# Kernel tuning notes

Hardware: AMD Instinct MI355X
Metric: run time of the kernel (lower is better)

## Reference

```python
import jax, jax.numpy as jnp
import numpy as np
import math

B, T, C, H = 2, 2048, 512, 8
K, DIL = 3, 1
EPS = 1e-5


def _ln(x, g, b):
    m = jnp.mean(x, axis=-1, keepdims=True)
    v = jnp.mean(jnp.square(x - m), axis=-1, keepdims=True)
    return (x - m) * jax.lax.rsqrt(v + EPS) * g + b


def setup_inputs() -> dict:
    key = jax.random.key(0)
    ks = jax.random.split(key, 12)
    s = 0.02
    return {
        "x": jax.random.normal(ks[0], (B, T, C), jnp.float32),
        "conv_w": jax.random.normal(ks[1], (C, C, K), jnp.float32) * s,  # OIH
        "conv_b": jax.random.normal(ks[2], (C,), jnp.float32) * s,
        "g1": jnp.ones((C,), jnp.float32), "b1": jnp.zeros((C,), jnp.float32),
        "qkv_w": jax.random.normal(ks[3], (C, 3 * C), jnp.float32) * s,
        "qkv_b": jax.random.normal(ks[4], (3 * C,), jnp.float32) * s,
        "proj_w": jax.random.normal(ks[5], (C, C), jnp.float32) * s,
        "proj_b": jax.random.normal(ks[6], (C,), jnp.float32) * s,
        "g2": jnp.ones((C,), jnp.float32), "b2": jnp.zeros((C,), jnp.float32),
        "ffn_w1": jax.random.normal(ks[7], (C, 2 * C), jnp.float32) * s,
        "ffn_b1": jax.random.normal(ks[8], (2 * C,), jnp.float32) * s,
        "ffn_w2": jax.random.normal(ks[9], (2 * C, C), jnp.float32) * s,
        "ffn_b2": jax.random.normal(ks[10], (C,), jnp.float32) * s,
        "g3": jnp.ones((C,), jnp.float32), "b3": jnp.zeros((C,), jnp.float32),
    }


def reference(x, conv_w, conv_b, g1, b1, qkv_w, qkv_b, proj_w, proj_b,
              g2, b2, ffn_w1, ffn_b1, ffn_w2, ffn_b2, g3, b3):
    b, t, c = x.shape
    hd = c // H
    # --- causal dilated conv (left-pad only == pad both + right-trim) ---
    pad = (K - 1) * DIL
    xc = jnp.transpose(x, (0, 2, 1))  # [B,C,T]
    conv = jax.lax.conv_general_dilated(
        xc, conv_w, window_strides=(1,), padding=[(pad, 0)],
        rhs_dilation=(DIL,), dimension_numbers=("NCH", "OIH", "NCH"))
    conv = conv + conv_b[None, :, None]
    x = _ln(x + jnp.transpose(conv, (0, 2, 1)), g1, b1)
    # --- causal self-attention ---
    qkv = (x @ qkv_w + qkv_b).reshape(b, t, 3, H, hd)
    qkv = jnp.transpose(qkv, (2, 0, 3, 1, 4))  # [3,B,H,T,hd]
    q, k, v = qkv[0], qkv[1], qkv[2]
    scores = jnp.einsum("bhqd,bhkd->bhqk", q, k) / math.sqrt(hd)
    causal = jnp.tril(jnp.ones((t, t), bool))
    scores = jnp.where(causal, scores, -jnp.inf)
    attn = jax.nn.softmax(scores, axis=-1)
    out = jnp.einsum("bhqk,bhkd->bhqd", attn, v)
    out = jnp.transpose(out, (0, 2, 1, 3)).reshape(b, t, c)
    out = out @ proj_w + proj_b
    x = _ln(x + out, g2, b2)
    # --- FFN ---
    ffn = jax.nn.relu(x @ ffn_w1 + ffn_b1) @ ffn_w2 + ffn_b2
    return _ln(x + ffn, g3, b3)
```

## Files before the change

### kernel.cpp

```cpp
#include <hip/hip_runtime.h>
#include <hip/hip_bf16.h>

#define TT 2048
#define QSC 0.18033688011112042f

typedef __attribute__((ext_vector_type(4))) float f32x4;
typedef __attribute__((ext_vector_type(8))) __bf16 bf16x8;
typedef __attribute__((ext_vector_type(4))) short short4v;
typedef __attribute__((ext_vector_type(8))) short short8v;

enum { M_CONV = 0, M_QKV = 1, M_PROJ = 2, M_FFN1 = 3, M_FFN2 = 4 };

__device__ __forceinline__ void gload16(const void* g, void* l) {
    __builtin_amdgcn_global_load_lds(
        (__attribute__((address_space(1))) void*)g,
        (__attribute__((address_space(3))) void*)l, 16, 0, 0);
}

__device__ __forceinline__ short f2bf(float f) {
    unsigned u = __float_as_uint(f);
    u = (u + 0x7fffu + ((u >> 16) & 1u)) >> 16;
    return (short)u;
}

__device__ __forceinline__ float bf2f(short s) {
    unsigned u = ((unsigned)(unsigned short)s) << 16;
    return __uint_as_float(u);
}

__global__ __launch_bounds__(256) void prep_all(
    const float* __restrict__ conv_w, const float* __restrict__ x,
    const float* __restrict__ qkv_w, const float* __restrict__ proj_w,
    const float* __restrict__ f1w, const float* __restrict__ f2w,
    short* __restrict__ cwT, short* __restrict__ xpad,
    short* __restrict__ qkvT, short* __restrict__ projT,
    short* __restrict__ f1T, short* __restrict__ f2T) {
    if (blockIdx.x < 2048) {
        int t = blockIdx.x;
        const float* src; short* dst; int K, N, lt;
        if (t < 768)       { src = qkv_w;  dst = qkvT;  K = 512;  N = 1536; lt = t; }
        else if (t < 1024) { src = proj_w; dst = projT; K = 512;  N = 512;  lt = t - 768; }
        else if (t < 1536) { src = f1w;    dst = f1T;   K = 512;  N = 1024; lt = t - 1024; }
        else               { src = f2w;    dst = f2T;   K = 1024; N = 512;  lt = t - 1536; }
        int ntn = N >> 5;
        int kt = lt / ntn, nt = lt - kt * ntn;
        int k0 = kt * 32, n0 = nt * 32;
        __shared__ float tile[32][33];
        int c = threadIdx.x & 31, r = threadIdx.x >> 5;
        #pragma unroll
        for (int i = 0; i < 4; i++)
            tile[r + i * 8][c] = src[(size_t)(k0 + r + i * 8) * N + n0 + c];
        __syncthreads();
        #pragma unroll
        for (int i = 0; i < 4; i++)
            dst[(size_t)(n0 + r + i * 8) * K + k0 + c] = f2bf(tile[c][r + i * 8]);
        return;
    }
    int idx = (blockIdx.x - 2048) * 256 + threadIdx.x;
    if (idx < 786432) {
        int tap = idx >> 18, i = (idx >> 9) & 511, o = idx & 511;
        cwT[(size_t)o * 1536 + tap * 512 + i] = f2bf(conv_w[((size_t)o * 512 + i) * 3 + tap]);
        return;
    }
    idx -= 786432;
    if (idx < 2099200) {
        int i = idx & 511, rp = idx >> 9;
        int bb = rp / 2050, rr = rp - bb * 2050;
        int t = rr - 2;
        float v = (t >= 0) ? x[((size_t)(bb << 11) + t) * 512 + i] : 0.f;
        xpad[((size_t)bb * 2050 + rr) * 512 + i] = f2bf(v);
    }
}

__global__ __launch_bounds__(512) void ln_row(const float* __restrict__ in,
                                              const float* __restrict__ g,
                                              const float* __restrict__ b,
                                              float* __restrict__ outf,
                                              short* __restrict__ outb) {
    int row = blockIdx.x * 8 + (threadIdx.x >> 6);
    int l = threadIdx.x & 63;
    const float* p = in + (size_t)row * 512 + l * 8;
    f32x4 v0 = *(const f32x4*)p;
    f32x4 v1 = *(const f32x4*)(p + 4);
    float s = 0.f, ss = 0.f;
    #pragma unroll
    for (int i = 0; i < 4; i++) { s += v0[i]; ss += v0[i] * v0[i]; }
    #pragma unroll
    for (int i = 0; i < 4; i++) { s += v1[i]; ss += v1[i] * v1[i]; }
    #pragma unroll
    for (int off = 1; off < 64; off <<= 1) {
        s  += __shfl_xor(s, off);
        ss += __shfl_xor(ss, off);
    }
    float mean = s * (1.f / 512);
    float var  = ss * (1.f / 512) - mean * mean;
    float rstd = rsqrtf(var + 1e-5f);
    f32x4 g0 = *(const f32x4*)(g + l * 8), g1 = *(const f32x4*)(g + l * 8 + 4);
    f32x4 b0 = *(const f32x4*)(b + l * 8), b1 = *(const f32x4*)(b + l * 8 + 4);
    f32x4 o0, o1;
    #pragma unroll
    for (int i = 0; i < 4; i++) {
        o0[i] = (v0[i] - mean) * rstd * g0[i] + b0[i];
        o1[i] = (v1[i] - mean) * rstd * g1[i] + b1[i];
    }
    float* q = outf + (size_t)row * 512 + l * 8;
    *(f32x4*)q = o0;
    *(f32x4*)(q + 4) = o1;
    if (outb) {
        short4v p0, p1;
        #pragma unroll
        for (int i = 0; i < 4; i++) { p0[i] = f2bf(o0[i]); p1[i] = f2bf(o1[i]); }
        *(short4v*)(outb + (size_t)row * 512 + l * 8) = p0;
        *(short4v*)(outb + (size_t)row * 512 + l * 8 + 4) = p1;
    }
}

template<int MODE>
__device__ __forceinline__ const short* a_ptr(const short* A, int m0, int r, int kk, int K) {
    if constexpr (MODE == M_CONV) {
        int row = m0 + r;
        int bb = row >> 11, t5 = row & 2047;
        int tap = kk >> 9, k2 = kk & 511;
        return A + ((size_t)(bb * 2050 + t5 + tap) * 512 + k2);
    } else {
        return A + ((size_t)(m0 + r) * K + kk);
    }
}

template<int MODE>
__global__ __launch_bounds__(128) void gemm_mfma(
    const short* __restrict__ A, const short* __restrict__ Bw,
    const float* __restrict__ bias, const float* __restrict__ res,
    void* __restrict__ Cout, short* __restrict__ vTb, int K) {
    __shared__ short As[64 * 64];
    __shared__ short Bs[64 * 64];
    const int tid = threadIdx.x;
    const int w = tid >> 6, l = tid & 63;
    const int lr = l & 15, lc = l >> 4;
    const int m0 = blockIdx.x * 64, n0 = blockIdx.y * 64;
    f32x4 acc[2][4];
    #pragma unroll
    for (int mf = 0; mf < 2; mf++)
        #pragma unroll
        for (int nf = 0; nf < 4; nf++) acc[mf][nf] = (f32x4){0.f, 0.f, 0.f, 0.f};

    for (int k0 = 0; k0 < K; k0 += 64) {
        #pragma unroll
        for (int i = 0; i < 4; i++) {
            int u = i * 128 + tid;
            int r = u >> 3, c = (u & 7) ^ (r & 7);
            gload16(a_ptr<MODE>(A, m0, r, k0 + c * 8, K), (char*)As + u * 16);
            gload16(Bw + ((size_t)(n0 + r) * K + k0 + c * 8), (char*)Bs + u * 16);
        }
        __syncthreads();
        bf16x8 af[2][2], bfv[4][2];
        #pragma unroll
        for (int mf = 0; mf < 2; mf++)
            #pragma unroll
            for (int ks = 0; ks < 2; ks++) {
                int rr = w * 32 + mf * 16 + lr;
                int cc = (ks * 4 + lc) ^ (rr & 7);
                af[mf][ks] = *(const bf16x8*)&As[rr * 64 + cc * 8];
            }
        #pragma unroll
        for (int nf = 0; nf < 4; nf++)
            #pragma unroll
            for (int ks = 0; ks < 2; ks++) {
                int rr = nf * 16 + lr;
                int cc = (ks * 4 + lc) ^ (rr & 7);
                bfv[nf][ks] = *(const bf16x8*)&Bs[rr * 64 + cc * 8];
            }
        __builtin_amdgcn_s_setprio(1);
        #pragma unroll
        for (int nf = 0; nf < 4; nf++)
            #pragma unroll
            for (int ks = 0; ks < 2; ks++)
                #pragma unroll
                for (int mf = 0; mf < 2; mf++)
                    acc[mf][nf] = __builtin_amdgcn_mfma_f32_16x16x32_bf16(
                        af[mf][ks], bfv[nf][ks], acc[mf][nf], 0, 0, 0);
        __builtin_amdgcn_s_setprio(0);
        __syncthreads();
    }
    #pragma unroll
    for (int mf = 0; mf < 2; mf++) {
        int row0 = m0 + w * 32 + mf * 16 + lc * 4;
        #pragma unroll
        for (int nf = 0; nf < 4; nf++) {
            int col = n0 + nf * 16 + lr;
            float bv = bias[col];
            if constexpr (MODE == M_CONV || MODE == M_PROJ || MODE == M_FFN2) {
                float* Cf = (float*)Cout;
                #pragma unroll
                for (int rg = 0; rg < 4; rg++) {
                    size_t off = (size_t)(row0 + rg) * 512 + col;
                    Cf[off] = acc[mf][nf][rg] + bv + res[off];
                }
            } else if constexpr (MODE == M_FFN1) {
                short* Cb = (short*)Cout;
                #pragma unroll
                for (int rg = 0; rg < 4; rg++)
                    Cb[(size_t)(row0 + rg) * 1024 + col] =
                        f2bf(fmaxf(acc[mf][nf][rg] + bv, 0.f));
            } else {
                short* Cb = (short*)Cout;
                float v[4];
                #pragma unroll
                for (int rg = 0; rg < 4; rg++) {
                    v[rg] = acc[mf][nf][rg] + bv;
                    float wv = (col < 512) ? v[rg] * QSC : v[rg];
                    Cb[(size_t)(row0 + rg) * 1536 + col] = f2bf(wv);
                }
                if (col >= 1024) {
                    int vc = col - 1024, hh = vc >> 6, dd = vc & 63;
                    int bb = row0 >> 11, t5 = row0 & 2047;
                    short4v pk = {f2bf(v[0]), f2bf(v[1]), f2bf(v[2]), f2bf(v[3])};
                    *(short4v*)&vTb[((size_t)((bb << 3) + hh) * 64 + dd) * 2048 + t5] = pk;
                }
            }
        }
    }
}

__global__ __launch_bounds__(256) void attn_part(const short* __restrict__ qkvb,
                                                 const short* __restrict__ vTb,
                                                 short* __restrict__ pO,
                                                 float* __restrict__ pML) {
    __shared__ short SM[20992];
    __bf16* SMb = (__bf16*)SM;
    const int tid = threadIdx.x;
    const int w = tid >> 6, l = tid & 63;
    const int lr = l & 15, lc = l >> 4;
    const int L = blockIdx.x;
    const int bh = L & 15;
    const int par = (L >> 4) & 1;
    const int qt = 31 - (L >> 5);
    const int b = bh >> 3, h = bh & 7;
    const int qr = w * 16, q0 = qt * 64;
    const int pbase = 16384 + w * (16 * 72);
    const int ntiles = (qt >= par) ? ((qt - par) >> 1) + 1 : 0;

    #pragma unroll
    for (int i = 0; i < 2; i++) {
        int u = i * 256 + tid, r = u >> 3, c = (u & 7) ^ (r & 7);
        gload16(qkvb + ((size_t)(b * 2048 + q0 + r) * 1536 + h * 64 + c * 8),
                (char*)&SM[16384] + u * 16);
        if (ntiles > 0) {
            gload16(qkvb + ((size_t)(b * 2048 + par * 64 + r) * 1536 + 512 + h * 64 + c * 8),
                    (char*)&SM[0] + u * 16);
            gload16(vTb + ((size_t)(bh * 64 + r) * 2048 + par * 64 + c * 8),
                    (char*)&SM[8192] + u * 16);
        }
    }
    __syncthreads();
    bf16x8 aq[2];
    #pragma unroll
    for (int ks = 0; ks < 2; ks++) {
        int rr = qr + lr;
        int cc = (lc + 4 * ks) ^ (rr & 7);
        aq[ks] = *(const bf16x8*)&SM[16384 + rr * 64 + cc * 8];
    }
    __syncthreads();

    bf16x8 onesf;
    #pragma unroll
    for (int i = 0; i < 8; i++) onesf[i] = (__bf16)1.0f;

    f32x4 o[4], lacc;
    float mst[4];
    #pragma unroll
    for (int nf = 0; nf < 4; nf++) o[nf] = (f32x4){0.f, 0.f, 0.f, 0.f};
    lacc = (f32x4){0.f, 0.f, 0.f, 0.f};
    #pragma unroll
    for (int rg = 0; rg < 4; rg++) mst[rg] = -1e30f;

    for (int s = 0; s < ntiles; s++) {
        const int kt = par + 2 * s;
        const int cur = s & 1;
        if (s + 1 < ntiles) {
            int ktn = kt + 2, nb = (cur ^ 1) * 4096;
            #pragma unroll
            for (int i = 0; i < 2; i++) {
                int u = i * 256 + tid, r = u >> 3, c = (u & 7) ^ (r & 7);
                gload16(qkvb + ((size_t)(b * 2048 + ktn * 64 + r) * 1536 + 512 + h * 64 + c * 8),
                        (char*)&SM[nb] + u * 16);
                gload16(vTb + ((size_t)(bh * 64 + r) * 2048 + ktn * 64 + c * 8),
                        (char*)&SM[8192 + nb] + u * 16);
            }
        }
        f32x4 s4[4];
        #pragma unroll
        for (int nf = 0; nf < 4; nf++) s4[nf] = (f32x4){0.f, 0.f, 0.f, 0.f};
        __builtin_amdgcn_s_setprio(1);
        #pragma unroll
        for (int nf = 0; nf < 4; nf++) {
            #pragma unroll
            for (int ks = 0; ks < 2; ks++) {
                int rr = nf * 16 + lr;
                int cc = (lc + 4 * ks) ^ (rr & 7);
                bf16x8 bk = *(const bf16x8*)&SM[cur * 4096 + rr * 64 + cc * 8];
                s4[nf] = __builtin_amdgcn_mfma_f32_16x16x32_bf16(aq[ks], bk, s4[nf], 0, 0, 0);
            }
        }
        __builtin_amdgcn_s_setprio(0);
        const bool diag = (kt == qt);
        if (diag) {
            #pragma unroll
            for (int nf = 0; nf < 4; nf++)
                #pragma unroll
                for (int rg = 0; rg < 4; rg++)
                    if (nf * 16 + lr > qr + lc * 4 + rg) s4[nf][rg] = -1e30f;
        }
        float rm[4];
        int ok = 1;
        #pragma unroll
        for (int rg = 0; rg < 4; rg++) {
            float m_ = fmaxf(fmaxf(s4[0][rg], s4[1][rg]), fmaxf(s4[2][rg], s4[3][rg]));
            m_ = fmaxf(m_, __shfl_xor(m_, 1));
            m_ = fmaxf(m_, __shfl_xor(m_, 2));
            m_ = fmaxf(m_, __shfl_xor(m_, 4));
            m_ = fmaxf(m_, __shfl_xor(m_, 8));
            rm[rg] = m_;
            ok &= (m_ <= mst[rg] + 11.5f);
        }
        if (!__all(ok)) {
            #pragma unroll
            for (int rg = 0; rg < 4; rg++) {
                float mn = fmaxf(mst[rg], rm[rg]);
                float alpha = exp2f(mst[rg] - mn);
                mst[rg] = mn;
                lacc[rg] *= alpha;
                #pragma unroll
                for (int nf = 0; nf < 4; nf++) o[nf][rg] *= alpha;
            }
        }
        #pragma unroll
        for (int rg = 0; rg < 4; rg++) {
            int prow = pbase + (lc * 4 + rg) * 72;
            SMb[prow      + lr] = (__bf16)exp2f(s4[0][rg] - mst[rg]);
            SMb[prow + 16 + lr] = (__bf16)exp2f(s4[1][rg] - mst[rg]);
            SMb[prow + 32 + lr] = (__bf16)exp2f(s4[2][rg] - mst[rg]);
            SMb[prow + 48 + lr] = (__bf16)exp2f(s4[3][rg] - mst[rg]);
        }
        bf16x8 pa[2];
        #pragma unroll
        for (int ks = 0; ks < 2; ks++)
            pa[ks] = *(const bf16x8*)&SM[pbase + lr * 72 + ks * 32 + lc * 8];
        __builtin_amdgcn_s_setprio(1);
        #pragma unroll
        for (int ks = 0; ks < 2; ks++)
            lacc = __builtin_amdgcn_mfma_f32_16x16x32_bf16(pa[ks], onesf, lacc, 0, 0, 0);
        #pragma unroll
        for (int nf = 0; nf < 4; nf++) {
            #pragma unroll
            for (int ks = 0; ks < 2; ks++) {
                int rr = nf * 16 + lr;
                int cc = (lc + 4 * ks) ^ (rr & 7);
                bf16x8 bv = *(const bf16x8*)&SM[8192 + cur * 4096 + rr * 64 + cc * 8];
                o[nf] = __builtin_amdgcn_mfma_f32_16x16x32_bf16(pa[ks], bv, o[nf], 0, 0, 0);
            }
        }
        __builtin_amdgcn_s_setprio(0);
        __syncthreads();
    }

    size_t ob = (size_t)L * 4096;
    #pragma unroll
    for (int nf = 0; nf < 4; nf++) {
        #pragma unroll
        for (int rg = 0; rg < 4; rg++) {
            int rw = qr + lc * 4 + rg;
            pO[ob + rw * 64 + nf * 16 + lr] = (ntiles > 0) ? f2bf(o[nf][rg]) : (short)0;
        }
    }
    if (lr == 0) {
        #pragma unroll
        for (int rg = 0; rg < 4; rg++) {
            int rw = qr + lc * 4 + rg;
            pML[(size_t)L * 128 + rw]      = (ntiles > 0) ? mst[rg] : -1e30f;
            pML[(size_t)L * 128 + 64 + rw] = (ntiles > 0) ? lacc[rg] : 0.f;
        }
    }
}

__global__ __launch_bounds__(256) void attn_merge(const short* __restrict__ pO,
                                                  const float* __restrict__ pML,
                                                  short* __restrict__ aout) {
    int U = blockIdx.x;
    int bh = U & 15, qt = U >> 4;
    int b = bh >> 3, h = bh & 7, q0 = qt * 64;
    int L0 = ((31 - qt) << 5) | bh;
    int L1 = L0 | 16;
    int t = threadIdx.x;
    int r = t >> 2, cs = (t & 3) * 16;
    float m0 = pML[(size_t)L0 * 128 + r], l0 = pML[(size_t)L0 * 128 + 64 + r];
    float m1 = pML[(size_t)L1 * 128 + r], l1 = pML[(size_t)L1 * 128 + 64 + r];
    float mn = fmaxf(m0, m1);
    float a0 = exp2f(m0 - mn), a1 = exp2f(m1 - mn);
    float inv = 1.f / (l0 * a0 + l1 * a1);
    #pragma unroll
    for (int half = 0; half < 2; half++) {
        int c0 = cs + half * 8;
        short8v o0 = *(const short8v*)&pO[(size_t)L0 * 4096 + r * 64 + c0];
        short8v o1 = *(const short8v*)&pO[(size_t)L1 * 4096 + r * 64 + c0];
        short8v ov;
        #pragma unroll
        for (int j = 0; j < 8; j++)
            ov[j] = f2bf((bf2f(o0[j]) * a0 + bf2f(o1[j]) * a1) * inv);
        *(short8v*)&aout[(size_t)(b * 2048 + q0 + r) * 512 + h * 64 + c0] = ov;
    }
}

extern "C" void kernel_launch(void* const* d_in, const int* in_sizes, int n_in,
                              void* d_out, int out_size, void* d_ws, size_t ws_size,
                              hipStream_t stream) {
    const float* x      = (const float*)d_in[0];
    const float* conv_w = (const float*)d_in[1];
    const float* conv_b = (const float*)d_in[2];
    const float* g1     = (const float*)d_in[3];
    const float* b1     = (const float*)d_in[4];
    const float* qkv_w  = (const float*)d_in[5];
    const float* qkv_b  = (const float*)d_in[6];
    const float* proj_w = (const float*)d_in[7];
    const float* proj_b = (const float*)d_in[8];
    const float* g2     = (const float*)d_in[9];
    const float* b2     = (const float*)d_in[10];
    const float* ffn_w1 = (const float*)d_in[11];
    const float* ffn_b1 = (const float*)d_in[12];
    const float* ffn_w2 = (const float*)d_in[13];
    const float* ffn_b2 = (const float*)d_in[14];
    const float* g3     = (const float*)d_in[15];
    const float* b3     = (const float*)d_in[16];
    float* out = (float*)d_out;

    char* p = (char*)d_ws;
    short* cwT   = (short*)p;  p += 786432 * 2;
    short* qkvT  = (short*)p;  p += 786432 * 2;
    short* projT = (short*)p;  p += 262144 * 2;
    short* f1T   = (short*)p;  p += 524288 * 2;
    short* f2T   = (short*)p;  p += 524288 * 2;
    short* xpad  = (short*)p;  p += 2099200 * 2;
    float* yb    = (float*)p;  p += 2097152 * 4;
    float* x1f   = (float*)p;  p += 2097152 * 4;
    short* x1b   = (short*)p;  p += 2097152 * 2;
    short* qkvb  = (short*)p;  p += 6291456 * 2;
    short* vTb   = (short*)p;  p += 2097152 * 2;
    short* pO    = (short*)p;  p += 4194304 * 2;
    float* pML   = (float*)p;  p += 131072 * 4;
    float* x2f     = x1f;
    short* x2b     = x1b;
    short* attnout = xpad;
    short* hb      = qkvb;

    prep_all<<<13320, 256, 0, stream>>>(conv_w, x, qkv_w, proj_w, ffn_w1, ffn_w2,
                                        cwT, xpad, qkvT, projT, f1T, f2T);
    gemm_mfma<M_CONV><<<dim3(64, 8), 128, 0, stream>>>(
        xpad, cwT, conv_b, x, yb, nullptr, 1536);
    ln_row<<<512, 512, 0, stream>>>(yb, g1, b1, x1f, x1b);
    gemm_mfma<M_QKV><<<dim3(64, 24), 128, 0, stream>>>(
        x1b, qkvT, qkv_b, nullptr, qkvb, vTb, 512);
    attn_part<<<1024, 256, 0, stream>>>(qkvb, vTb, pO, pML);
    attn_merge<<<512, 256, 0, stream>>>(pO, pML, attnout);
    gemm_mfma<M_PROJ><<<dim3(64, 8), 128, 0, stream>>>(
        attnout, projT, proj_b, x1f, yb, nullptr, 512);
    ln_row<<<512, 512, 0, stream>>>(yb, g2, b2, x2f, x2b);
    gemm_mfma<M_FFN1><<<dim3(64, 16), 128, 0, stream>>>(
        x2b, f1T, ffn_b1, nullptr, hb, nullptr, 512);
    gemm_mfma<M_FFN2><<<dim3(64, 8), 128, 0, stream>>>(
        hb, f2T, ffn_b2, x2f, yb, nullptr, 1024);
    ln_row<<<512, 512, 0, stream>>>(yb, g3, b3, out, nullptr);
}
```

Baseline: 135.6 us.

## Fuse attention merge into proj GEMM A-load and store intermediates in bf16

Removes the separate attn_merge kernel. The proj GEMM now merges the two partial attention outputs, using their max and sum statistics, while staging its A tile into shared memory. All residual and pre-LayerNorm intermediates (yb, x1, x2) are stored as bf16 instead of fp32, which roughly halves their memory traffic and drops one launch. The costs are lower residual precision and a synchronous register-path A load in the proj GEMM instead of async global-to-LDS loads.

```diff
diff --git a/kernel.cpp b/kernel.cpp
--- a/kernel.cpp
+++ b/kernel.cpp
@@ -72,21 +72,21 @@
     }
 }
 
-__global__ __launch_bounds__(512) void ln_row(const float* __restrict__ in,
+__global__ __launch_bounds__(512) void ln_row(const short* __restrict__ in,
                                               const float* __restrict__ g,
                                               const float* __restrict__ b,
                                               float* __restrict__ outf,
                                               short* __restrict__ outb) {
     int row = blockIdx.x * 8 + (threadIdx.x >> 6);
     int l = threadIdx.x & 63;
-    const float* p = in + (size_t)row * 512 + l * 8;
-    f32x4 v0 = *(const f32x4*)p;
-    f32x4 v1 = *(const f32x4*)(p + 4);
+    short8v v = *(const short8v*)(in + (size_t)row * 512 + l * 8);
+    float vf[8];
     float s = 0.f, ss = 0.f;
     #pragma unroll
-    for (int i = 0; i < 4; i++) { s += v0[i]; ss += v0[i] * v0[i]; }
-    #pragma unroll
-    for (int i = 0; i < 4; i++) { s += v1[i]; ss += v1[i] * v1[i]; }
+    for (int i = 0; i < 8; i++) {
+        vf[i] = bf2f(v[i]);
+        s += vf[i]; ss += vf[i] * vf[i];
+    }
     #pragma unroll
     for (int off = 1; off < 64; off <<= 1) {
         s  += __shfl_xor(s, off);
@@ -97,21 +97,22 @@
     float rstd = rsqrtf(var + 1e-5f);
     f32x4 g0 = *(const f32x4*)(g + l * 8), g1 = *(const f32x4*)(g + l * 8 + 4);
     f32x4 b0 = *(const f32x4*)(b + l * 8), b1 = *(const f32x4*)(b + l * 8 + 4);
-    f32x4 o0, o1;
+    float ov[8];
     #pragma unroll
     for (int i = 0; i < 4; i++) {
-        o0[i] = (v0[i] - mean) * rstd * g0[i] + b0[i];
-        o1[i] = (v1[i] - mean) * rstd * g1[i] + b1[i];
-    }
-    float* q = outf + (size_t)row * 512 + l * 8;
-    *(f32x4*)q = o0;
-    *(f32x4*)(q + 4) = o1;
+        ov[i]     = (vf[i]     - mean) * rstd * g0[i] + b0[i];
+        ov[i + 4] = (vf[i + 4] - mean) * rstd * g1[i] + b1[i];
+    }
+    if (outf) {
+        float* q = outf + (size_t)row * 512 + l * 8;
+        *(f32x4*)q       = (f32x4){ov[0], ov[1], ov[2], ov[3]};
+        *(f32x4*)(q + 4) = (f32x4){ov[4], ov[5], ov[6], ov[7]};
+    }
     if (outb) {
-        short4v p0, p1;
-        #pragma unroll
-        for (int i = 0; i < 4; i++) { p0[i] = f2bf(o0[i]); p1[i] = f2bf(o1[i]); }
-        *(short4v*)(outb + (size_t)row * 512 + l * 8) = p0;
-        *(short4v*)(outb + (size_t)row * 512 + l * 8 + 4) = p1;
+        short8v pk;
+        #pragma unroll
+        for (int i = 0; i < 8; i++) pk[i] = f2bf(ov[i]);
+        *(short8v*)(outb + (size_t)row * 512 + l * 8) = pk;
     }
 }
 
@@ -130,8 +131,9 @@
 template<int MODE>
 __global__ __launch_bounds__(128) void gemm_mfma(
     const short* __restrict__ A, const short* __restrict__ Bw,
-    const float* __restrict__ bias, const float* __restrict__ res,
-    void* __restrict__ Cout, short* __restrict__ vTb, int K) {
+    const float* __restrict__ bias, const void* __restrict__ res,
+    void* __restrict__ Cout, short* __restrict__ vTb,
+    const float* __restrict__ pML, int K) {
     __shared__ short As[64 * 64];
     __shared__ short Bs[64 * 64];
     const int tid = threadIdx.x;
@@ -145,12 +147,41 @@
         for (int nf = 0; nf < 4; nf++) acc[mf][nf] = (f32x4){0.f, 0.f, 0.f, 0.f};
 
     for (int k0 = 0; k0 < K; k0 += 64) {
-        #pragma unroll
-        for (int i = 0; i < 4; i++) {
-            int u = i * 128 + tid;
-            int r = u >> 3, c = (u & 7) ^ (r & 7);
-            gload16(a_ptr<MODE>(A, m0, r, k0 + c * 8, K), (char*)As + u * 16);
-            gload16(Bw + ((size_t)(n0 + r) * K + k0 + c * 8), (char*)Bs + u * 16);
+        if constexpr (MODE == M_PROJ) {
+            const int bq = blockIdx.x >> 5, qt = blockIdx.x & 31;
+            const int h = k0 >> 6;
+            const int Lb = ((31 - qt) << 5) | (bq * 8 + h);
+            #pragma unroll
+            for (int i = 0; i < 4; i++) {
+                int u = i * 128 + tid, r = u >> 3, c = (u & 7) ^ (r & 7);
+                float m0_ = pML[(size_t)Lb * 128 + r];
+                float l0_ = pML[(size_t)Lb * 128 + 64 + r];
+                float m1_ = pML[(size_t)(Lb | 16) * 128 + r];
+                float l1_ = pML[(size_t)(Lb | 16) * 128 + 64 + r];
+                float mn = fmaxf(m0_, m1_);
+                float a0 = exp2f(m0_ - mn), a1 = exp2f(m1_ - mn);
+                float inv = 1.f / (l0_ * a0 + l1_ * a1);
+                short8v o0 = *(const short8v*)&A[(size_t)Lb * 4096 + r * 64 + c * 8];
+                short8v o1 = *(const short8v*)&A[(size_t)(Lb | 16) * 4096 + r * 64 + c * 8];
+                short8v mv;
+                #pragma unroll
+                for (int j = 0; j < 8; j++)
+                    mv[j] = f2bf((bf2f(o0[j]) * a0 + bf2f(o1[j]) * a1) * inv);
+                *(short8v*)((char*)As + u * 16) = mv;
+            }
+            #pragma unroll
+            for (int i = 0; i < 4; i++) {
+                int u = i * 128 + tid, r = u >> 3, c = (u & 7) ^ (r & 7);
+                gload16(Bw + ((size_t)(n0 + r) * K + k0 + c * 8), (char*)Bs + u * 16);
+            }
+        } else {
+            #pragma unroll
+            for (int i = 0; i < 4; i++) {
+                int u = i * 128 + tid;
+                int r = u >> 3, c = (u & 7) ^ (r & 7);
+                gload16(a_ptr<MODE>(A, m0, r, k0 + c * 8, K), (char*)As + u * 16);
+                gload16(Bw + ((size_t)(n0 + r) * K + k0 + c * 8), (char*)Bs + u * 16);
+            }
         }
         __syncthreads();
         bf16x8 af[2][2], bfv[4][2];
@@ -189,12 +220,21 @@
         for (int nf = 0; nf < 4; nf++) {
             int col = n0 + nf * 16 + lr;
             float bv = bias[col];
-            if constexpr (MODE == M_CONV || MODE == M_PROJ || MODE == M_FFN2) {
-                float* Cf = (float*)Cout;
+            if constexpr (MODE == M_CONV) {
+                short* Cb = (short*)Cout;
+                const float* rf = (const float*)res;
                 #pragma unroll
                 for (int rg = 0; rg < 4; rg++) {
                     size_t off = (size_t)(row0 + rg) * 512 + col;
-                    Cf[off] = acc[mf][nf][rg] + bv + res[off];
+                    Cb[off] = f2bf(acc[mf][nf][rg] + bv + rf[off]);
+                }
+            } else if constexpr (MODE == M_PROJ || MODE == M_FFN2) {
+                short* Cb = (short*)Cout;
+                const short* rb = (const short*)res;
+                #pragma unroll
+                for (int rg = 0; rg < 4; rg++) {
+                    size_t off = (size_t)(row0 + rg) * 512 + col;
+                    Cb[off] = f2bf(acc[mf][nf][rg] + bv + bf2f(rb[off]));
                 }
             } else if constexpr (MODE == M_FFN1) {
                 short* Cb = (short*)Cout;
@@ -380,34 +420,6 @@
             pML[(size_t)L * 128 + rw]      = (ntiles > 0) ? mst[rg] : -1e30f;
             pML[(size_t)L * 128 + 64 + rw] = (ntiles > 0) ? lacc[rg] : 0.f;
         }
-    }
-}
-
-__global__ __launch_bounds__(256) void attn_merge(const short* __restrict__ pO,
-                                                  const float* __restrict__ pML,
-                                                  short* __restrict__ aout) {
-    int U = blockIdx.x;
-    int bh = U & 15, qt = U >> 4;
-    int b = bh >> 3, h = bh & 7, q0 = qt * 64;
-    int L0 = ((31 - qt) << 5) | bh;
-    int L1 = L0 | 16;
-    int t = threadIdx.x;
-    int r = t >> 2, cs = (t & 3) * 16;
-    float m0 = pML[(size_t)L0 * 128 + r], l0 = pML[(size_t)L0 * 128 + 64 + r];
-    float m1 = pML[(size_t)L1 * 128 + r], l1 = pML[(size_t)L1 * 128 + 64 + r];
-    float mn = fmaxf(m0, m1);
-    float a0 = exp2f(m0 - mn), a1 = exp2f(m1 - mn);
-    float inv = 1.f / (l0 * a0 + l1 * a1);
-    #pragma unroll
-    for (int half = 0; half < 2; half++) {
-        int c0 = cs + half * 8;
-        short8v o0 = *(const short8v*)&pO[(size_t)L0 * 4096 + r * 64 + c0];
-        short8v o1 = *(const short8v*)&pO[(size_t)L1 * 4096 + r * 64 + c0];
-        short8v ov;
-        #pragma unroll
-        for (int j = 0; j < 8; j++)
-            ov[j] = f2bf((bf2f(o0[j]) * a0 + bf2f(o1[j]) * a1) * inv);
-        *(short8v*)&aout[(size_t)(b * 2048 + q0 + r) * 512 + h * 64 + c0] = ov;
     }
 }
 
@@ -440,33 +452,29 @@
     short* f1T   = (short*)p;  p += 524288 * 2;
     short* f2T   = (short*)p;  p += 524288 * 2;
     short* xpad  = (short*)p;  p += 2099200 * 2;
-    float* yb    = (float*)p;  p += 2097152 * 4;
-    float* x1f   = (float*)p;  p += 2097152 * 4;
+    short* yb    = (short*)p;  p += 2097152 * 2;
     short* x1b   = (short*)p;  p += 2097152 * 2;
     short* qkvb  = (short*)p;  p += 6291456 * 2;
     short* vTb   = (short*)p;  p += 2097152 * 2;
     short* pO    = (short*)p;  p += 4194304 * 2;
     float* pML   = (float*)p;  p += 131072 * 4;
-    float* x2f     = x1f;
-    short* x2b     = x1b;
-    short* attnout = xpad;
-    short* hb      = qkvb;
+    short* x2b = x1b;
+    short* hb  = qkvb;
 
     prep_all<<<13320, 256, 0, stream>>>(conv_w, x, qkv_w, proj_w, ffn_w1, ffn_w2,
                                         cwT, xpad, qkvT, projT, f1T, f2T);
     gemm_mfma<M_CONV><<<dim3(64, 8), 128, 0, stream>>>(
-        xpad, cwT, conv_b, x, yb, nullptr, 1536);
-    ln_row<<<512, 512, 0, stream>>>(yb, g1, b1, x1f, x1b);
+        xpad, cwT, conv_b, x, yb, nullptr, nullptr, 1536);
+    ln_row<<<512, 512, 0, stream>>>(yb, g1, b1, nullptr, x1b);
     gemm_mfma<M_QKV><<<dim3(64, 24), 128, 0, stream>>>(
-        x1b, qkvT, qkv_b, nullptr, qkvb, vTb, 512);
+        x1b, qkvT, qkv_b, nullptr, qkvb, vTb, nullptr, 512);
     attn_part<<<1024, 256, 0, stream>>>(qkvb, vTb, pO, pML);
-    attn_merge<<<512, 256, 0, stream>>>(pO, pML, attnout);
     gemm_mfma<M_PROJ><<<dim3(64, 8), 128, 0, stream>>>(
-        attnout, projT, proj_b, x1f, yb, nullptr, 512);
-    ln_row<<<512, 512, 0, stream>>>(yb, g2, b2, x2f, x2b);
+        pO, projT, proj_b, x1b, yb, nullptr, pML, 512);
+    ln_row<<<512, 512, 0, stream>>>(yb, g2, b2, nullptr, x2b);
     gemm_mfma<M_FFN1><<<dim3(64, 16), 128, 0, stream>>>(
-        x2b, f1T, ffn_b1, nullptr, hb, nullptr, 512);
+        x2b, f1T, ffn_b1, nullptr, hb, nullptr, nullptr, 512);
     gemm_mfma<M_FFN2><<<dim3(64, 8), 128, 0, stream>>>(
-        hb, f2T, ffn_b2, x2f, yb, nullptr, 1024);
+        hb, f2T, ffn_b2, x2b, yb, nullptr, nullptr, 1024);
     ln_row<<<512, 512, 0, stream>>>(yb, g3, b3, out, nullptr);
 }
```

After: 134.6 us. Within noise of the previous version (-0.7%).
